# Kernel optimization log

Hardware: AMD Instinct MI355X
Metric: run time of the kernel (lower is better)

The kernel has to match this reference:

```python
import jax, jax.numpy as jnp
import numpy as np

B, S, D, H = 32, 8192, 128, 128


def setup_inputs() -> dict:
    key = jax.random.key(0)
    ks = jax.random.split(key, 8)
    x = jax.random.normal(ks[0], (B, D), dtype=jnp.float32)
    context = jax.random.normal(ks[1], (B, S, D), dtype=jnp.float32)
    mask = jax.random.bernoulli(ks[2], 0.3, (B, S))
    mask = mask.at[:, 0].set(False)
    W_in = jax.random.normal(ks[3], (H, D), dtype=jnp.float32) / np.sqrt(D)
    b_in = jax.random.normal(ks[4], (H,), dtype=jnp.float32) * 0.01
    # torch Conv1d(D, H, 1) weight is [H, D, 1]; squeeze kernel dim -> [H, D]
    W_ctx = jax.random.normal(ks[5], (H, D), dtype=jnp.float32) / np.sqrt(D)
    b_ctx = jax.random.normal(ks[6], (H,), dtype=jnp.float32) * 0.01
    V = jax.random.uniform(ks[7], (H,), dtype=jnp.float32, minval=-1.0, maxval=1.0)
    return {"x": x, "context": context, "mask": mask, "W_in": W_in,
            "b_in": b_in, "W_ctx": W_ctx, "b_ctx": b_ctx, "V": V}


def reference(x, context, mask, W_in, b_in, W_ctx, b_ctx, V):
    # x: [B, D] decoder hidden state; context: [B, S, D]; mask: [B, S] bool (True = masked)
    inp = x @ W_in.T + b_in                                  # [B, H]
    # Conv1d with kernel size 1 == pointwise linear over D
    ctx = jnp.einsum('bsd,hd->bhs', context, W_ctx) + b_ctx[None, :, None]  # [B, H, S]
    att = jnp.einsum('h,bhs->bs', V, jnp.tanh(inp[:, :, None] + ctx))       # [B, S]
    att = jnp.where(mask, -jnp.inf, att)
    alpha = jax.nn.softmax(att, axis=1)                      # [B, S]
    hidden_state = jnp.einsum('bhs,bs->bh', ctx, alpha)      # [B, H]
    return hidden_state, att
```

## Files before the change

### kernel.cpp

```cpp
#include <hip/hip_runtime.h>
#include <math.h>

#define BB 32
#define SS 8192
#define DD 128
#define HH 128
#define TS 128
#define RH 136

#define MASK_NEG (-1e30f)

typedef _Float16 half8 __attribute__((ext_vector_type(8)));
typedef _Float16 half4 __attribute__((ext_vector_type(4)));
typedef float f32x4 __attribute__((ext_vector_type(4)));

__global__ __launch_bounds__(128) void k_inp(const float* __restrict__ x,
                                             const float* __restrict__ W_in,
                                             const float* __restrict__ b_in,
                                             const float* __restrict__ b_ctx,
                                             float* __restrict__ inp2) {
    int b = blockIdx.x;
    int h = threadIdx.x;
    const float* xr = x + b * DD;
    const float* wr = W_in + h * DD;
    float a0 = 0.f, a1 = 0.f, a2 = 0.f, a3 = 0.f;
#pragma unroll
    for (int d = 0; d < DD; d += 4) {
        a0 = fmaf(xr[d + 0], wr[d + 0], a0);
        a1 = fmaf(xr[d + 1], wr[d + 1], a1);
        a2 = fmaf(xr[d + 2], wr[d + 2], a2);
        a3 = fmaf(xr[d + 3], wr[d + 3], a3);
    }
    inp2[b * HH + h] = b_in[h] + b_ctx[h] + ((a0 + a1) + (a2 + a3));
}

__global__ __launch_bounds__(256) void k_wsplit(const float* __restrict__ W_ctx,
                                                _Float16* __restrict__ Whi,
                                                _Float16* __restrict__ Wlo) {
    int i = blockIdx.x * 256 + threadIdx.x;
    float w = W_ctx[i];
    _Float16 hi = (_Float16)w;
    Whi[i] = hi;
    Wlo[i] = (_Float16)(w - (float)hi);
}

__global__ __launch_bounds__(256, 2) void k_att(const float* __restrict__ context,
                                                const unsigned char* __restrict__ mask,
                                                const _Float16* __restrict__ Whi,
                                                const _Float16* __restrict__ Wlo,
                                                const float* __restrict__ V,
                                                const float* __restrict__ inp2,
                                                float* __restrict__ att_out) {
    const int b = blockIdx.y;
    const int s0 = blockIdx.x * TS;
    const int tid = threadIdx.x;

    __shared__ _Float16 Chi[TS * RH];
    __shared__ _Float16 Clo[TS * RH];
    __shared__ float red[4][TS];

    {
        const float4* src = (const float4*)(context + ((size_t)b * SS + s0) * DD);
#pragma unroll
        for (int i = 0; i < 16; ++i) {
            int f = i * 256 + tid;
            int row = f >> 5;
            int c4 = f & 31;
            float4 v = src[f];
            half4 hv, lv;
            hv.x = (_Float16)v.x; lv.x = (_Float16)(v.x - (float)hv.x);
            hv.y = (_Float16)v.y; lv.y = (_Float16)(v.y - (float)hv.y);
            hv.z = (_Float16)v.z; lv.z = (_Float16)(v.z - (float)hv.z);
            hv.w = (_Float16)v.w; lv.w = (_Float16)(v.w - (float)hv.w);
            *(half4*)&Chi[row * RH + c4 * 4] = hv;
            *(half4*)&Clo[row * RH + c4 * 4] = lv;
        }
    }
    __syncthreads();

    const int wv = tid >> 6;
    const int lane = tid & 63;
    const int ln = lane & 15;
    const int quad = lane >> 4;
    const int m0 = wv * 32;

    f32x4 acc[2][8];
#pragma unroll
    for (int mt = 0; mt < 2; ++mt)
#pragma unroll
        for (int nt = 0; nt < 8; ++nt) acc[mt][nt] = (f32x4){0.f, 0.f, 0.f, 0.f};

    const _Float16* aH = Whi + (size_t)(m0 + ln) * DD;
    const _Float16* aL = Wlo + (size_t)(m0 + ln) * DD;

#pragma unroll
    for (int ks = 0; ks < 4; ++ks) {
        const int k0 = ks * 32 + quad * 8;
        half8 aH0 = *(const half8*)(aH + k0);
        half8 aH1 = *(const half8*)(aH + 16 * DD + k0);
        half8 aL0 = *(const half8*)(aL + k0);
        half8 aL1 = *(const half8*)(aL + 16 * DD + k0);
#pragma unroll
        for (int nt = 0; nt < 8; ++nt) {
            const int srow = nt * 16 + ln;
            half8 bH = *(const half8*)&Chi[srow * RH + k0];
            half8 bL = *(const half8*)&Clo[srow * RH + k0];
            acc[0][nt] = __builtin_amdgcn_mfma_f32_16x16x32_f16(aH0, bH, acc[0][nt], 0, 0, 0);
            acc[0][nt] = __builtin_amdgcn_mfma_f32_16x16x32_f16(aL0, bH, acc[0][nt], 0, 0, 0);
            acc[0][nt] = __builtin_amdgcn_mfma_f32_16x16x32_f16(aH0, bL, acc[0][nt], 0, 0, 0);
            acc[1][nt] = __builtin_amdgcn_mfma_f32_16x16x32_f16(aH1, bH, acc[1][nt], 0, 0, 0);
            acc[1][nt] = __builtin_amdgcn_mfma_f32_16x16x32_f16(aL1, bH, acc[1][nt], 0, 0, 0);
            acc[1][nt] = __builtin_amdgcn_mfma_f32_16x16x32_f16(aH1, bL, acc[1][nt], 0, 0, 0);
        }
    }

    float bias[8], vv[8];
    const float* ib = inp2 + b * HH;
#pragma unroll
    for (int j = 0; j < 8; ++j) {
        int h = m0 + (j >> 2) * 16 + quad * 4 + (j & 3);
        bias[j] = ib[h];
        vv[j] = V[h];
    }
#pragma unroll
    for (int nt = 0; nt < 8; ++nt) {
        float p = 0.f;
#pragma unroll
        for (int j = 0; j < 8; ++j) {
            float sc = acc[j >> 2][nt][j & 3] + bias[j];
            p = fmaf(vv[j], tanhf(sc), p);
        }
        p += __shfl_xor(p, 16);
        p += __shfl_xor(p, 32);
        if (quad == 0) red[wv][nt * 16 + ln] = p;
    }
    __syncthreads();

    if (tid < TS) {
        float att = red[0][tid] + red[1][tid] + red[2][tid] + red[3][tid];
        size_t idx = (size_t)b * SS + s0 + tid;
        if (mask[idx]) att = MASK_NEG;
        att_out[idx] = att;
    }
}

__global__ __launch_bounds__(1024) void k_softmax(const float* __restrict__ att,
                                                  float* __restrict__ alpha) {
    const int b = blockIdx.x;
    const int t = threadIdx.x;
    const float* arow = att + (size_t)b * SS;
    float v[SS / 1024];
    float m = -INFINITY;
#pragma unroll
    for (int i = 0; i < SS / 1024; ++i) {
        v[i] = arow[t + 1024 * i];
        m = fmaxf(m, v[i]);
    }
#pragma unroll
    for (int off = 32; off; off >>= 1) m = fmaxf(m, __shfl_xor(m, off));
    __shared__ float redm[16];
    const int wave = t >> 6;
    if ((t & 63) == 0) redm[wave] = m;
    __syncthreads();
    {
        float mm = redm[t & 15];
#pragma unroll
        for (int off = 8; off; off >>= 1) mm = fmaxf(mm, __shfl_xor(mm, off));
        m = mm;
    }

    float e[SS / 1024];
    float sum = 0.f;
#pragma unroll
    for (int i = 0; i < SS / 1024; ++i) {
        e[i] = expf(v[i] - m);
        sum += e[i];
    }
#pragma unroll
    for (int off = 32; off; off >>= 1) sum += __shfl_xor(sum, off);
    __shared__ float reds[16];
    if ((t & 63) == 0) reds[wave] = sum;
    __syncthreads();
    {
        float ss = reds[t & 15];
#pragma unroll
        for (int off = 8; off; off >>= 1) ss += __shfl_xor(ss, off);
        sum = ss;
    }

    const float inv = 1.0f / sum;
    float* arowo = alpha + (size_t)b * SS;
#pragma unroll
    for (int i = 0; i < SS / 1024; ++i) arowo[t + 1024 * i] = e[i] * inv;
}

__global__ __launch_bounds__(256) void k_cbar(const float* __restrict__ context,
                                              const float* __restrict__ alpha,
                                              float* __restrict__ cbar) {
    const int b = blockIdx.y;
    const int d4 = threadIdx.x & 31;
    const int sl = threadIdx.x >> 5;
    const int s0 = blockIdx.x * 1024;
    const float4* cb = (const float4*)(context + (size_t)b * SS * DD);
    const float* al = alpha + (size_t)b * SS;
    float4 acc = make_float4(0.f, 0.f, 0.f, 0.f);
#pragma unroll 4
    for (int s = s0 + sl; s < s0 + 1024; s += 8) {
        float a = al[s];
        float4 v = cb[(size_t)s * (DD / 4) + d4];
        acc.x = fmaf(a, v.x, acc.x);
        acc.y = fmaf(a, v.y, acc.y);
        acc.z = fmaf(a, v.z, acc.z);
        acc.w = fmaf(a, v.w, acc.w);
    }
    __shared__ float4 sm[256];
    sm[threadIdx.x] = acc;
    __syncthreads();
    if (threadIdx.x < 32) {
        float4 r = sm[threadIdx.x];
#pragma unroll
        for (int j = 1; j < 8; ++j) {
            float4 tv = sm[threadIdx.x + 32 * j];
            r.x += tv.x;
            r.y += tv.y;
            r.z += tv.z;
            r.w += tv.w;
        }
        atomicAdd(&cbar[b * DD + 4 * d4 + 0], r.x);
        atomicAdd(&cbar[b * DD + 4 * d4 + 1], r.y);
        atomicAdd(&cbar[b * DD + 4 * d4 + 2], r.z);
        atomicAdd(&cbar[b * DD + 4 * d4 + 3], r.w);
    }
}

__global__ __launch_bounds__(256) void k_hidden(const float* __restrict__ cbar,
                                                const float* __restrict__ W_ctx,
                                                const float* __restrict__ b_ctx,
                                                float* __restrict__ hidden) {
    const int idx = blockIdx.x * 256 + threadIdx.x;
    const int b = idx >> 7;
    const int h = idx & 127;
    const float* cb = cbar + b * DD;
    const float* w = W_ctx + h * DD;
    float a0 = 0.f, a1 = 0.f, a2 = 0.f, a3 = 0.f;
#pragma unroll
    for (int d = 0; d < DD; d += 4) {
        a0 = fmaf(cb[d + 0], w[d + 0], a0);
        a1 = fmaf(cb[d + 1], w[d + 1], a1);
        a2 = fmaf(cb[d + 2], w[d + 2], a2);
        a3 = fmaf(cb[d + 3], w[d + 3], a3);
    }
    hidden[b * HH + h] = b_ctx[h] + ((a0 + a1) + (a2 + a3));
}

extern "C" void kernel_launch(void* const* d_in, const int* in_sizes, int n_in,
                              void* d_out, int out_size, void* d_ws, size_t ws_size,
                              hipStream_t stream) {
    const float* x = (const float*)d_in[0];
    const float* context = (const float*)d_in[1];
    const unsigned char* mask = (const unsigned char*)d_in[2];
    const float* W_in = (const float*)d_in[3];
    const float* b_in = (const float*)d_in[4];
    const float* W_ctx = (const float*)d_in[5];
    const float* b_ctx = (const float*)d_in[6];
    const float* V = (const float*)d_in[7];

    float* out = (float*)d_out;
    float* hidden = out;
    float* att = out + BB * HH;

    float* ws = (float*)d_ws;
    float* inp2 = ws;
    float* alpha = inp2 + BB * HH;
    float* cbar = alpha + (size_t)BB * SS;
    _Float16* Whi = (_Float16*)(cbar + BB * DD);
    _Float16* Wlo = Whi + HH * DD;

    hipMemsetAsync(cbar, 0, BB * DD * sizeof(float), stream);

    k_wsplit<<<dim3(DD * HH / 256), dim3(256), 0, stream>>>(W_ctx, Whi, Wlo);
    k_inp<<<dim3(BB), dim3(HH), 0, stream>>>(x, W_in, b_in, b_ctx, inp2);
    k_att<<<dim3(SS / TS, BB), dim3(256), 0, stream>>>(context, mask, Whi, Wlo, V, inp2,
                                                       att);
    k_softmax<<<dim3(BB), dim3(1024), 0, stream>>>(att, alpha);
    k_cbar<<<dim3(SS / 1024, BB), dim3(256), 0, stream>>>(context, alpha, cbar);
    k_hidden<<<dim3(BB * HH / 256), dim3(256), 0, stream>>>(cbar, W_ctx, b_ctx, hidden);
}
```

Before: 281.1 us.

## Drop LDS staging in k_att, load context directly into MFMA operands

Each wave now loads its own 32 context rows straight from global memory into registers and splits them into fp16 hi/lo operands, instead of staging the whole tile in LDS with a block-wide barrier. W fragments are read from global memory (L2-resident) per M tile. The per-wave reduction writes att directly, so the shared reduction buffer and both barriers go away, and occupancy is raised to 4 blocks per CU. It also swaps tanhf for an exp-based fast tanh and gives k_cbar four times as many blocks for more parallelism. The risks are heavier repeated global W loads per wave and lower accuracy near the tanh saturation edges.

```diff
diff --git a/kernel.cpp b/kernel.cpp
--- a/kernel.cpp
+++ b/kernel.cpp
@@ -6,13 +6,16 @@
 #define DD 128
 #define HH 128
 #define TS 128
-#define RH 136
 
 #define MASK_NEG (-1e30f)
 
 typedef _Float16 half8 __attribute__((ext_vector_type(8)));
-typedef _Float16 half4 __attribute__((ext_vector_type(4)));
 typedef float f32x4 __attribute__((ext_vector_type(4)));
+
+__device__ __forceinline__ float fast_tanh(float x) {
+    float t = __expf(2.0f * x);
+    return 1.0f - 2.0f / (t + 1.0f);
+}
 
 __global__ __launch_bounds__(128) void k_inp(const float* __restrict__ x,
                                              const float* __restrict__ W_in,
@@ -44,7 +47,21 @@
     Wlo[i] = (_Float16)(w - (float)hi);
 }
 
-__global__ __launch_bounds__(256, 2) void k_att(const float* __restrict__ context,
+__device__ __forceinline__ void split8(const float4 a, const float4 b, half8& hi,
+                                       half8& lo) {
+    float f0 = a.x, f1 = a.y, f2 = a.z, f3 = a.w;
+    float f4 = b.x, f5 = b.y, f6 = b.z, f7 = b.w;
+    hi[0] = (_Float16)f0; lo[0] = (_Float16)(f0 - (float)hi[0]);
+    hi[1] = (_Float16)f1; lo[1] = (_Float16)(f1 - (float)hi[1]);
+    hi[2] = (_Float16)f2; lo[2] = (_Float16)(f2 - (float)hi[2]);
+    hi[3] = (_Float16)f3; lo[3] = (_Float16)(f3 - (float)hi[3]);
+    hi[4] = (_Float16)f4; lo[4] = (_Float16)(f4 - (float)hi[4]);
+    hi[5] = (_Float16)f5; lo[5] = (_Float16)(f5 - (float)hi[5]);
+    hi[6] = (_Float16)f6; lo[6] = (_Float16)(f6 - (float)hi[6]);
+    hi[7] = (_Float16)f7; lo[7] = (_Float16)(f7 - (float)hi[7]);
+}
+
+__global__ __launch_bounds__(256, 4) void k_att(const float* __restrict__ context,
                                                 const unsigned char* __restrict__ mask,
                                                 const _Float16* __restrict__ Whi,
                                                 const _Float16* __restrict__ Wlo,
@@ -53,94 +70,69 @@
                                                 float* __restrict__ att_out) {
     const int b = blockIdx.y;
     const int s0 = blockIdx.x * TS;
-    const int tid = threadIdx.x;
-
-    __shared__ _Float16 Chi[TS * RH];
-    __shared__ _Float16 Clo[TS * RH];
-    __shared__ float red[4][TS];
-
-    {
-        const float4* src = (const float4*)(context + ((size_t)b * SS + s0) * DD);
-#pragma unroll
-        for (int i = 0; i < 16; ++i) {
-            int f = i * 256 + tid;
-            int row = f >> 5;
-            int c4 = f & 31;
-            float4 v = src[f];
-            half4 hv, lv;
-            hv.x = (_Float16)v.x; lv.x = (_Float16)(v.x - (float)hv.x);
-            hv.y = (_Float16)v.y; lv.y = (_Float16)(v.y - (float)hv.y);
-            hv.z = (_Float16)v.z; lv.z = (_Float16)(v.z - (float)hv.z);
-            hv.w = (_Float16)v.w; lv.w = (_Float16)(v.w - (float)hv.w);
-            *(half4*)&Chi[row * RH + c4 * 4] = hv;
-            *(half4*)&Clo[row * RH + c4 * 4] = lv;
-        }
-    }
-    __syncthreads();
-
-    const int wv = tid >> 6;
-    const int lane = tid & 63;
+    const int wv = threadIdx.x >> 6;
+    const int lane = threadIdx.x & 63;
     const int ln = lane & 15;
     const int quad = lane >> 4;
-    const int m0 = wv * 32;
-
-    f32x4 acc[2][8];
-#pragma unroll
-    for (int mt = 0; mt < 2; ++mt)
-#pragma unroll
-        for (int nt = 0; nt < 8; ++nt) acc[mt][nt] = (f32x4){0.f, 0.f, 0.f, 0.f};
-
-    const _Float16* aH = Whi + (size_t)(m0 + ln) * DD;
-    const _Float16* aL = Wlo + (size_t)(m0 + ln) * DD;
+    const int sw = s0 + wv * 32;
+
+    f32x4 acc[8][2];
+#pragma unroll
+    for (int mt = 0; mt < 8; ++mt) {
+        acc[mt][0] = (f32x4){0.f, 0.f, 0.f, 0.f};
+        acc[mt][1] = (f32x4){0.f, 0.f, 0.f, 0.f};
+    }
+
+    const float* crow0 = context + ((size_t)b * SS + sw + ln) * DD;
+    const float* crow1 = crow0 + 16 * DD;
 
 #pragma unroll
     for (int ks = 0; ks < 4; ++ks) {
         const int k0 = ks * 32 + quad * 8;
-        half8 aH0 = *(const half8*)(aH + k0);
-        half8 aH1 = *(const half8*)(aH + 16 * DD + k0);
-        half8 aL0 = *(const half8*)(aL + k0);
-        half8 aL1 = *(const half8*)(aL + 16 * DD + k0);
-#pragma unroll
-        for (int nt = 0; nt < 8; ++nt) {
-            const int srow = nt * 16 + ln;
-            half8 bH = *(const half8*)&Chi[srow * RH + k0];
-            half8 bL = *(const half8*)&Clo[srow * RH + k0];
-            acc[0][nt] = __builtin_amdgcn_mfma_f32_16x16x32_f16(aH0, bH, acc[0][nt], 0, 0, 0);
-            acc[0][nt] = __builtin_amdgcn_mfma_f32_16x16x32_f16(aL0, bH, acc[0][nt], 0, 0, 0);
-            acc[0][nt] = __builtin_amdgcn_mfma_f32_16x16x32_f16(aH0, bL, acc[0][nt], 0, 0, 0);
-            acc[1][nt] = __builtin_amdgcn_mfma_f32_16x16x32_f16(aH1, bH, acc[1][nt], 0, 0, 0);
-            acc[1][nt] = __builtin_amdgcn_mfma_f32_16x16x32_f16(aL1, bH, acc[1][nt], 0, 0, 0);
-            acc[1][nt] = __builtin_amdgcn_mfma_f32_16x16x32_f16(aH1, bL, acc[1][nt], 0, 0, 0);
+        float4 b0a = *(const float4*)(crow0 + k0);
+        float4 b0b = *(const float4*)(crow0 + k0 + 4);
+        float4 b1a = *(const float4*)(crow1 + k0);
+        float4 b1b = *(const float4*)(crow1 + k0 + 4);
+        half8 bH0, bL0, bH1, bL1;
+        split8(b0a, b0b, bH0, bL0);
+        split8(b1a, b1b, bH1, bL1);
+#pragma unroll
+        for (int mt = 0; mt < 8; ++mt) {
+            const size_t aoff = (size_t)(mt * 16 + ln) * DD + k0;
+            half8 aH = *(const half8*)(Whi + aoff);
+            half8 aL = *(const half8*)(Wlo + aoff);
+            acc[mt][0] = __builtin_amdgcn_mfma_f32_16x16x32_f16(aH, bH0, acc[mt][0], 0, 0, 0);
+            acc[mt][0] = __builtin_amdgcn_mfma_f32_16x16x32_f16(aL, bH0, acc[mt][0], 0, 0, 0);
+            acc[mt][0] = __builtin_amdgcn_mfma_f32_16x16x32_f16(aH, bL0, acc[mt][0], 0, 0, 0);
+            acc[mt][1] = __builtin_amdgcn_mfma_f32_16x16x32_f16(aH, bH1, acc[mt][1], 0, 0, 0);
+            acc[mt][1] = __builtin_amdgcn_mfma_f32_16x16x32_f16(aL, bH1, acc[mt][1], 0, 0, 0);
+            acc[mt][1] = __builtin_amdgcn_mfma_f32_16x16x32_f16(aH, bL1, acc[mt][1], 0, 0, 0);
         }
     }
 
-    float bias[8], vv[8];
     const float* ib = inp2 + b * HH;
-#pragma unroll
-    for (int j = 0; j < 8; ++j) {
-        int h = m0 + (j >> 2) * 16 + quad * 4 + (j & 3);
-        bias[j] = ib[h];
-        vv[j] = V[h];
-    }
-#pragma unroll
-    for (int nt = 0; nt < 8; ++nt) {
-        float p = 0.f;
-#pragma unroll
-        for (int j = 0; j < 8; ++j) {
-            float sc = acc[j >> 2][nt][j & 3] + bias[j];
-            p = fmaf(vv[j], tanhf(sc), p);
+    float p0 = 0.f, p1 = 0.f;
+#pragma unroll
+    for (int mt = 0; mt < 8; ++mt) {
+#pragma unroll
+        for (int j = 0; j < 4; ++j) {
+            const int h = mt * 16 + quad * 4 + j;
+            const float bias = ib[h];
+            const float vj = V[h];
+            p0 = fmaf(vj, fast_tanh(acc[mt][0][j] + bias), p0);
+            p1 = fmaf(vj, fast_tanh(acc[mt][1][j] + bias), p1);
         }
-        p += __shfl_xor(p, 16);
-        p += __shfl_xor(p, 32);
-        if (quad == 0) red[wv][nt * 16 + ln] = p;
-    }
-    __syncthreads();
-
-    if (tid < TS) {
-        float att = red[0][tid] + red[1][tid] + red[2][tid] + red[3][tid];
-        size_t idx = (size_t)b * SS + s0 + tid;
-        if (mask[idx]) att = MASK_NEG;
-        att_out[idx] = att;
+    }
+    p0 += __shfl_xor(p0, 16);
+    p0 += __shfl_xor(p0, 32);
+    p1 += __shfl_xor(p1, 16);
+    p1 += __shfl_xor(p1, 32);
+
+    if (quad == 0) {
+        const size_t i0 = (size_t)b * SS + sw + ln;
+        att_out[i0] = mask[i0] ? MASK_NEG : p0;
+        const size_t i1 = i0 + 16;
+        att_out[i1] = mask[i1] ? MASK_NEG : p1;
     }
 }
 
@@ -200,12 +192,12 @@
     const int b = blockIdx.y;
     const int d4 = threadIdx.x & 31;
     const int sl = threadIdx.x >> 5;
-    const int s0 = blockIdx.x * 1024;
+    const int s0 = blockIdx.x * 256;
     const float4* cb = (const float4*)(context + (size_t)b * SS * DD);
     const float* al = alpha + (size_t)b * SS;
     float4 acc = make_float4(0.f, 0.f, 0.f, 0.f);
 #pragma unroll 4
-    for (int s = s0 + sl; s < s0 + 1024; s += 8) {
+    for (int s = s0 + sl; s < s0 + 256; s += 8) {
         float a = al[s];
         float4 v = cb[(size_t)s * (DD / 4) + d4];
         acc.x = fmaf(a, v.x, acc.x);
@@ -283,6 +275,6 @@
     k_att<<<dim3(SS / TS, BB), dim3(256), 0, stream>>>(context, mask, Whi, Wlo, V, inp2,
                                                        att);
     k_softmax<<<dim3(BB), dim3(1024), 0, stream>>>(att, alpha);
-    k_cbar<<<dim3(SS / 1024, BB), dim3(256), 0, stream>>>(context, alpha, cbar);
+    k_cbar<<<dim3(SS / 256, BB), dim3(256), 0, stream>>>(context, alpha, cbar);
     k_hidden<<<dim3(BB * HH / 256), dim3(256), 0, stream>>>(cbar, W_ctx, b_ctx, hidden);
 }
```

Measured after the change: 321.0 us. +14.2%, slower.
